# Optimization experiments

Measured on AMD Instinct MI355X. Metric: run time of the kernel, lower is better.

Reference implementation:

```python
import jax, jax.numpy as jnp
import numpy as np

P_DROP = 0.1
KEEP = 1.0 - P_DROP


def setup_inputs() -> dict:
    key = jax.random.key(0)
    ks = jax.random.split(key, 8)
    N, E, D, H, O, L = 50000, 800000, 128, 128, 64, 3
    x = jax.random.normal(ks[0], (N, D), dtype=jnp.float32)
    edge_index = jax.random.randint(ks[1], (2, E), 0, N, dtype=jnp.int64)
    s = 0.05  # weight scale for numeric stability
    Ws1 = jax.random.normal(ks[2], (L, D, H), dtype=jnp.float32) * s
    bs1 = jnp.zeros((L, H), dtype=jnp.float32)
    Ws2 = jax.random.normal(ks[3], (L, H, H), dtype=jnp.float32) * s
    bs2 = jnp.zeros((L, H), dtype=jnp.float32)
    Wlin = jax.random.normal(ks[4], (H, O), dtype=jnp.float32) * s
    blin = jnp.zeros((O,), dtype=jnp.float32)
    return {"x": x, "edge_index": edge_index, "Ws1": Ws1, "bs1": bs1,
            "Ws2": Ws2, "bs2": bs2, "Wlin": Wlin, "blin": blin}


def _gin_conv(x, src, dst, W1, b1, W2, b2, n_nodes):
    # GINConv (eps=0): h = MLP(x + sum_{j in N(i)} x_j)
    agg = jax.ops.segment_sum(x[src], dst, num_segments=n_nodes)  # [N, D]
    h = x + agg
    h = jax.nn.relu(h @ W1 + b1)
    h = jax.nn.relu(h @ W2 + b2)
    return h


def reference(x, edge_index, Ws1, bs1, Ws2, bs2, Wlin, blin):
    n_nodes = x.shape[0]
    src, dst = edge_index[0], edge_index[1]  # PyG flow: message from src to dst
    L = Ws1.shape[0]
    dkeys = jax.random.split(jax.random.key(42), L)
    h = x
    for l in range(L):
        h = _gin_conv(h, src, dst, Ws1[l], bs1[l], Ws2[l], bs2[l], n_nodes)
        h = jax.nn.relu(h)
        mask = jax.random.bernoulli(dkeys[l], KEEP, h.shape)
        h = jnp.where(mask, h / KEEP, 0.0)  # dropout p=0.1, training=True
    return h @ Wlin + blin
```

## Files before the change

kernel.cpp:

```cpp
#include <hip/hip_runtime.h>
#include <stdint.h>

typedef short short8 __attribute__((ext_vector_type(8)));
typedef float float4v __attribute__((ext_vector_type(4)));

__device__ static inline unsigned short f2bf(float f) {
  uint32_t u = __float_as_uint(f);
  u += 0x7fffu + ((u >> 16) & 1u);
  return (unsigned short)(u >> 16);
}
__device__ static inline float bf_lo(uint32_t v) { return __uint_as_float(v << 16); }
__device__ static inline float bf_hi(uint32_t v) { return __uint_as_float(v & 0xffff0000u); }

__host__ __device__ static inline void tf2x32(uint32_t k0, uint32_t k1,
                                              uint32_t x0, uint32_t x1,
                                              uint32_t* o0, uint32_t* o1) {
  const uint32_t ks2 = k0 ^ k1 ^ 0x1BD11BDAu;
  x0 += k0; x1 += k1;
#define TF_RND(r) { x0 += x1; x1 = (x1 << (r)) | (x1 >> (32 - (r))); x1 ^= x0; }
  TF_RND(13) TF_RND(15) TF_RND(26) TF_RND(6)
  x0 += k1;  x1 += ks2 + 1u;
  TF_RND(17) TF_RND(29) TF_RND(16) TF_RND(24)
  x0 += ks2; x1 += k0 + 2u;
  TF_RND(13) TF_RND(15) TF_RND(26) TF_RND(6)
  x0 += k0;  x1 += k1 + 3u;
  TF_RND(17) TF_RND(29) TF_RND(16) TF_RND(24)
  x0 += k1;  x1 += ks2 + 4u;
  TF_RND(13) TF_RND(15) TF_RND(26) TF_RND(6)
  x0 += ks2; x1 += k0 + 5u;
#undef TF_RND
  *o0 = x0; *o1 = x1;
}

__device__ static inline bool tf_keep(uint32_t k0, uint32_t k1, uint32_t idx) {
  uint32_t o0, o1;
  tf2x32(k0, k1, 0u, idx, &o0, &o1);
  const uint32_t bits = o0 ^ o1;
  const float u = __uint_as_float((bits >> 9) | 0x3f800000u) - 1.0f;
  return u < 0.9f;
}

__device__ static inline uint32_t mask_word(uint32_t k0, uint32_t k1, int b, int t) {
  const int wave = t >> 6, lane = t & 63;
  const int ch = wave & 1, rtw = wave >> 1;
  const int m = lane & 15, kg = lane >> 4;
  const int node0 = b * 64;
  uint32_t km = 0;
#pragma unroll
  for (int rt = 0; rt < 2; ++rt) {
#pragma unroll
    for (int nt = 0; nt < 4; ++nt) {
      const int col = ch * 64 + nt * 16 + m;
#pragma unroll
      for (int r = 0; r < 4; ++r) {
        const int ro = node0 + (rtw * 2 + rt) * 16 + kg * 4 + r;
        if (tf_keep(k0, k1, (uint32_t)ro * 128u + (uint32_t)col))
          km |= 1u << (rt * 16 + nt * 4 + r);
      }
    }
  }
  return km;
}

__global__ __launch_bounds__(256) void prep_kernel(
    const int* __restrict__ dst, int* __restrict__ count8, int N, int E,
    const float* __restrict__ x, unsigned short* __restrict__ xb,
    unsigned short* __restrict__ xb2, int n4,
    const float* __restrict__ Ws1, const float* __restrict__ Ws2,
    const float* __restrict__ Wlin, unsigned short* __restrict__ wpack,
    uint32_t* __restrict__ mask, int lblocks,
    uint32_t dk00, uint32_t dk01,
    int nCnt, int nConv, int nI) {
  const int t = threadIdx.x;
  const int g = blockIdx.x;
  if (g >= 10 * nI) {
    const int tid = (g - 10 * nI) * 256 + t;
    if (tid >= 13312) return;
    const float* W;
    int cols, r;
    size_t obase;
    if (tid < 12288) {
      const int mm = tid / 2048;
      r = tid % 2048;
      const int l = mm >> 1;
      W = (mm & 1) ? (Ws2 + (size_t)l * 16384) : (Ws1 + (size_t)l * 16384);
      cols = 128;
      obase = (size_t)mm * 16384;
    } else {
      r = tid - 12288;
      W = Wlin;
      cols = 64;
      obase = 6 * 16384;
    }
    const int ch = (cols == 128) ? (r >> 10) : 0;
    const int kt = (r >> 8) & 3;
    const int nt = (r >> 6) & 3;
    const int lane = r & 63;
    const int n = ch * 64 + nt * 16 + (lane & 15);
    const int kbase = kt * 32 + (lane >> 4) * 8;
    unsigned short o[8];
#pragma unroll
    for (int j = 0; j < 8; ++j) o[j] = f2bf(W[(size_t)(kbase + j) * cols + n]);
    uint4 ov;
    ov.x = (uint32_t)o[0] | ((uint32_t)o[1] << 16);
    ov.y = (uint32_t)o[2] | ((uint32_t)o[3] << 16);
    ov.z = (uint32_t)o[4] | ((uint32_t)o[5] << 16);
    ov.w = (uint32_t)o[6] | ((uint32_t)o[7] << 16);
    *(uint4*)(wpack + obase + ((size_t)((ch * 16 + kt * 4 + nt) * 64 + lane)) * 8) = ov;
    return;
  }
  const int cls = g % 10;
  const int j = g / 10;
  if (cls == 0) {
    if (j >= nCnt) return;
    const int tid = j * 256 + t;
    const int nt4 = (E + 3) >> 2;
    if (tid >= nt4) return;
    int* cseg = count8 + (size_t)(j & 7) * N;
    const int base = tid * 4;
    if (base + 4 <= E) {
      const int4 d4 = ((const int4*)dst)[tid];
      atomicAdd(&cseg[d4.x], 1);
      atomicAdd(&cseg[d4.y], 1);
      atomicAdd(&cseg[d4.z], 1);
      atomicAdd(&cseg[d4.w], 1);
    } else {
      for (int k = base; k < E; ++k) atomicAdd(&cseg[dst[k]], 1);
    }
    return;
  }
  if (cls == 9) {
    if (j >= lblocks) return;
    mask[(size_t)j * 256 + t] = mask_word(dk00, dk01, j, t);
    return;
  }
  const int cb = j * 8 + (cls - 1);
  if (cb >= nConv) return;
  const int i = cb * 256 + t;
  if (i < n4) {
    const float4 v = ((const float4*)x)[i];
    uint2 o;
    o.x = (uint32_t)f2bf(v.x) | ((uint32_t)f2bf(v.y) << 16);
    o.y = (uint32_t)f2bf(v.z) | ((uint32_t)f2bf(v.w) << 16);
    ((uint2*)xb)[i] = o;
  } else if (i < n4 + 32) {
    uint2 z; z.x = 0u; z.y = 0u;
    ((uint2*)xb)[i] = z;
    ((uint2*)xb2)[i] = z;
  }
}

__global__ __launch_bounds__(256) void scan1_kernel(
    const int* __restrict__ count8, int* __restrict__ bsum, int M8) {
  __shared__ int red[4];
  const int i = blockIdx.x * 256 + threadIdx.x;
  int v = (i < M8) ? count8[i] : 0;
  for (int off = 32; off > 0; off >>= 1) v += __shfl_down(v, off, 64);
  if ((threadIdx.x & 63) == 0) red[threadIdx.x >> 6] = v;
  __syncthreads();
  if (threadIdx.x == 0) bsum[blockIdx.x] = red[0] + red[1] + red[2] + red[3];
}

__global__ __launch_bounds__(256) void scan2_kernel(int* __restrict__ bsum, int nb) {
  __shared__ int buf[256];
  __shared__ int carry_s;
  const int t = threadIdx.x;
  if (t == 0) carry_s = 0;
  __syncthreads();
  for (int base = 0; base < nb; base += 256) {
    const int c = carry_s;
    const int i = base + t;
    const int v = (i < nb) ? bsum[i] : 0;
    __syncthreads();
    buf[t] = v;
    __syncthreads();
    for (int off = 1; off < 256; off <<= 1) {
      const int add = (t >= off) ? buf[t - off] : 0;
      __syncthreads();
      buf[t] += add;
      __syncthreads();
    }
    if (i < nb) bsum[i] = c + ((t == 0) ? 0 : buf[t - 1]);
    if (t == 0) carry_s = c + buf[255];
    __syncthreads();
  }
}

__global__ __launch_bounds__(256) void scan3_kernel(
    const int* __restrict__ count8, const int* __restrict__ bsum,
    int* __restrict__ cursor8, int M8) {
  __shared__ int buf[256];
  const int t = threadIdx.x;
  const int i = blockIdx.x * 256 + t;
  const int c = (i < M8) ? count8[i] : 0;
  buf[t] = c;
  __syncthreads();
  for (int off = 1; off < 256; off <<= 1) {
    const int add = (t >= off) ? buf[t - off] : 0;
    __syncthreads();
    buf[t] += add;
    __syncthreads();
  }
  if (i < M8) cursor8[i] = bsum[blockIdx.x] + buf[t] - c;
}

__global__ __launch_bounds__(256) void fill8_kernel(
    const int* __restrict__ src, const int* __restrict__ dst,
    int* __restrict__ cursor8, int* __restrict__ csr, int N, int E,
    uint32_t* __restrict__ mask, int lblocks,
    uint32_t dk10, uint32_t dk11, uint32_t dk20, uint32_t dk21, int nFill) {
  const int t = threadIdx.x;
  const int cls = blockIdx.x % 3;
  const int j = blockIdx.x / 3;
  if (cls == 0) {
    if (j >= nFill) return;
    const int tid = j * 256 + t;
    const int nt4 = (E + 3) >> 2;
    if (tid >= nt4) return;
    int* cseg = cursor8 + (size_t)(j & 7) * N;
    const int base = tid * 4;
    if (base + 4 <= E) {
      const int4 s4 = ((const int4*)src)[tid];
      const int4 d4 = ((const int4*)dst)[tid];
      const int p0 = atomicAdd(&cseg[d4.x], 1);
      const int p1 = atomicAdd(&cseg[d4.y], 1);
      const int p2 = atomicAdd(&cseg[d4.z], 1);
      const int p3 = atomicAdd(&cseg[d4.w], 1);
      csr[p0] = s4.x; csr[p1] = s4.y; csr[p2] = s4.z; csr[p3] = s4.w;
    } else {
      for (int k = base; k < E; ++k) {
        const int pos = atomicAdd(&cseg[dst[k]], 1);
        csr[pos] = src[k];
      }
    }
    return;
  }
  if (j >= lblocks) return;
  const uint32_t k0 = (cls == 1) ? dk10 : dk20;
  const uint32_t k1 = (cls == 1) ? dk11 : dk21;
  mask[(size_t)cls * lblocks * 256 + (size_t)j * 256 + t] = mask_word(k0, k1, j, t);
}

#define ACC16(vv, A0,A1,A2,A3,A4,A5,A6,A7)                         \
  A0 += bf_lo(vv.x); A1 += bf_hi(vv.x); A2 += bf_lo(vv.y); A3 += bf_hi(vv.y); \
  A4 += bf_lo(vv.z); A5 += bf_hi(vv.z); A6 += bf_lo(vv.w); A7 += bf_hi(vv.w);

__global__ __launch_bounds__(256, 3) void gin_layer_kernel(
    const unsigned short* __restrict__ hIn, unsigned short* __restrict__ hOut,
    const int* __restrict__ csr, const int* __restrict__ cursor8,
    const int* __restrict__ count8,
    const unsigned short* __restrict__ W1p, const float* __restrict__ b1,
    const unsigned short* __restrict__ W2p, const float* __restrict__ b2,
    const uint32_t* __restrict__ maskL, int N, int E) {
  __shared__ __align__(16) unsigned short agg[64 * 136];
  __shared__ __align__(16) unsigned short t1[64 * 136];
  const int t = threadIdx.x;
  const int q = t & 15;
  const int gb = (t & 63) & 48;
  const int node0 = blockIdx.x * 64;
  const uint4* hv = (const uint4*)hIn;

  for (int p = 0; p < 4; ++p) {
    const int nn = p * 16 + (t >> 4);
    const int node = node0 + nn;
    if (node < N) {
      int oe = 0, ol = 0;
      if (q < 8) {
        oe = cursor8[(size_t)q * N + node];
        ol = count8[(size_t)q * N + node];
      }
      int b0, b1s, b2s, b3s, b4s, b5s, b6s, b7s;
      int l0, l1, l2, l3, l4, l5, l6, l7;
      {
        int e;
        e = __shfl(oe, gb + 0, 64); l0 = __shfl(ol, gb + 0, 64); b0  = e - l0;
        e = __shfl(oe, gb + 1, 64); l1 = __shfl(ol, gb + 1, 64); b1s = e - l1;
        e = __shfl(oe, gb + 2, 64); l2 = __shfl(ol, gb + 2, 64); b2s = e - l2;
        e = __shfl(oe, gb + 3, 64); l3 = __shfl(ol, gb + 3, 64); b3s = e - l3;
        e = __shfl(oe, gb + 4, 64); l4 = __shfl(ol, gb + 4, 64); b4s = e - l4;
        e = __shfl(oe, gb + 5, 64); l5 = __shfl(ol, gb + 5, 64); b5s = e - l5;
        e = __shfl(oe, gb + 6, 64); l6 = __shfl(ol, gb + 6, 64); b6s = e - l6;
        e = __shfl(oe, gb + 7, 64); l7 = __shfl(ol, gb + 7, 64); b7s = e - l7;
      }
      const int c1 = l0, c2 = c1 + l1, c3 = c2 + l2, c4 = c3 + l3;
      const int c5 = c4 + l4, c6 = c5 + l5, c7 = c6 + l6, T = c7 + l7;

      const uint4 sv = hv[(size_t)node * 16 + q];
      float a0 = bf_lo(sv.x), a1 = bf_hi(sv.x), a2 = bf_lo(sv.y), a3 = bf_hi(sv.y);
      float a4 = bf_lo(sv.z), a5 = bf_hi(sv.z), a6 = bf_lo(sv.w), a7 = bf_hi(sv.w);
      float d0 = 0.f, d1 = 0.f, d2 = 0.f, d3 = 0.f, d4 = 0.f, d5 = 0.f, d6 = 0.f, d7 = 0.f;

      for (int base = 0; base < T; base += 16) {
        const int j = base + q;
        int pos = b0 + j;
        pos = (j >= c1) ? (b1s + j - c1) : pos;
        pos = (j >= c2) ? (b2s + j - c2) : pos;
        pos = (j >= c3) ? (b3s + j - c3) : pos;
        pos = (j >= c4) ? (b4s + j - c4) : pos;
        pos = (j >= c5) ? (b5s + j - c5) : pos;
        pos = (j >= c6) ? (b6s + j - c6) : pos;
        pos = (j >= c7) ? (b7s + j - c7) : pos;
        pos = (pos < E) ? pos : (E - 1);
        const int idx = (j < T) ? csr[pos] : N;
        uint4 v[16];
#pragma unroll
        for (int jj = 0; jj < 16; ++jj) {
          const int s = __shfl(idx, gb + jj, 64);
          v[jj] = hv[(size_t)s * 16 + q];
        }
#pragma unroll
        for (int jj = 0; jj < 16; jj += 2) {
          ACC16(v[jj], a0, a1, a2, a3, a4, a5, a6, a7)
          ACC16(v[jj + 1], d0, d1, d2, d3, d4, d5, d6, d7)
        }
      }
      a0 += d0; a1 += d1; a2 += d2; a3 += d3;
      a4 += d4; a5 += d5; a6 += d6; a7 += d7;

      uint4 ov;
      ov.x = (uint32_t)f2bf(a0) | ((uint32_t)f2bf(a1) << 16);
      ov.y = (uint32_t)f2bf(a2) | ((uint32_t)f2bf(a3) << 16);
      ov.z = (uint32_t)f2bf(a4) | ((uint32_t)f2bf(a5) << 16);
      ov.w = (uint32_t)f2bf(a6) | ((uint32_t)f2bf(a7) << 16);
      *(uint4*)(agg + (size_t)nn * 136 + q * 8) = ov;
    }
  }
  __syncthreads();

  const int wave = t >> 6, lane = t & 63;
  const int ch = wave & 1;
  const int rtw = wave >> 1;
  const int m = lane & 15, kg = lane >> 4;

  short8 bfrag[16];
  {
    const short8* wp = (const short8*)W1p + (size_t)(ch * 16) * 64 + lane;
#pragma unroll
    for (int i = 0; i < 16; ++i) bfrag[i] = wp[(size_t)i * 64];
  }
  float4v acc[2][4] = {};
#pragma unroll
  for (int rt = 0; rt < 2; ++rt) {
    const int lrow = (rtw * 2 + rt) * 16 + m;
#pragma unroll
    for (int kt = 0; kt < 4; ++kt) {
      const short8 af = *(const short8*)(agg + (size_t)lrow * 136 + kt * 32 + kg * 8);
#pragma unroll
      for (int nt = 0; nt < 4; ++nt)
        acc[rt][nt] = __builtin_amdgcn_mfma_f32_16x16x32_bf16(
            af, bfrag[kt * 4 + nt], acc[rt][nt], 0, 0, 0);
    }
  }
#pragma unroll
  for (int rt = 0; rt < 2; ++rt) {
#pragma unroll
    for (int nt = 0; nt < 4; ++nt) {
      const int col = ch * 64 + nt * 16 + m;
      const float bb = b1[col];
#pragma unroll
      for (int r = 0; r < 4; ++r) {
        const int lrow = (rtw * 2 + rt) * 16 + kg * 4 + r;
        float v = acc[rt][nt][r] + bb;
        v = fmaxf(v, 0.0f);
        t1[(size_t)lrow * 136 + col] = f2bf(v);
      }
    }
  }
  __syncthreads();

  {
    const short8* wp = (const short8*)W2p + (size_t)(ch * 16) * 64 + lane;
#pragma unroll
    for (int i = 0; i < 16; ++i) bfrag[i] = wp[(size_t)i * 64];
  }
  float4v acc2[2][4] = {};
#pragma unroll
  for (int rt = 0; rt < 2; ++rt) {
    const int lrow = (rtw * 2 + rt) * 16 + m;
#pragma unroll
    for (int kt = 0; kt < 4; ++kt) {
      const short8 af = *(const short8*)(t1 + (size_t)lrow * 136 + kt * 32 + kg * 8);
#pragma unroll
      for (int nt = 0; nt < 4; ++nt)
        acc2[rt][nt] = __builtin_amdgcn_mfma_f32_16x16x32_bf16(
            af, bfrag[kt * 4 + nt], acc2[rt][nt], 0, 0, 0);
    }
  }
  const uint32_t km = maskL[(size_t)blockIdx.x * 256 + t];
  const float KEEP_INV = 1.0f / 0.9f;
#pragma unroll
  for (int rt = 0; rt < 2; ++rt) {
#pragma unroll
    for (int nt = 0; nt < 4; ++nt) {
      const int col = ch * 64 + nt * 16 + m;
      const float bb = b2[col];
#pragma unroll
      for (int r = 0; r < 4; ++r) {
        const int lrow = (rtw * 2 + rt) * 16 + kg * 4 + r;
        float v = acc2[rt][nt][r] + bb;
        v = fmaxf(v, 0.0f);
        v = ((km >> (rt * 16 + nt * 4 + r)) & 1u) ? v * KEEP_INV : 0.0f;
        agg[(size_t)lrow * 136 + col] = f2bf(v);
      }
    }
  }
  __syncthreads();

  const int orow = t >> 2;
  const int oc0 = (t & 3) * 8;
  const int gnode = node0 + orow;
  if (gnode < N) {
#pragma unroll
    for (int i = 0; i < 4; ++i) {
      const uint4 vv = *(const uint4*)(agg + (size_t)orow * 136 + oc0 + i * 32);
      *(uint4*)(hOut + (size_t)gnode * 128 + oc0 + i * 32) = vv;
    }
  }
}

__global__ __launch_bounds__(256) void final_gemm_kernel(
    const unsigned short* __restrict__ A, const unsigned short* __restrict__ Wp,
    const float* __restrict__ bias, float* __restrict__ out, int M) {
  const int wave = threadIdx.x >> 6;
  const int lane = threadIdx.x & 63;
  const int m = lane & 15;
  const int kg = lane >> 4;

  short8 bfrag[16];
  const short8* wp = (const short8*)Wp + lane;
#pragma unroll
  for (int i = 0; i < 16; ++i) bfrag[i] = wp[(size_t)i * 64];

  const int row0 = blockIdx.x * 64 + wave * 16;
  const int arow = (row0 + m < M) ? (row0 + m) : (M - 1);
  const short8* ap = (const short8*)(A + (size_t)arow * 128 + kg * 8);

  short8 afrag[4];
#pragma unroll
  for (int kt = 0; kt < 4; ++kt) afrag[kt] = ap[kt * 4];

  float4v acc[4] = {};
#pragma unroll
  for (int kt = 0; kt < 4; ++kt) {
#pragma unroll
    for (int nt = 0; nt < 4; ++nt)
      acc[nt] = __builtin_amdgcn_mfma_f32_16x16x32_bf16(
          afrag[kt], bfrag[kt * 4 + nt], acc[nt], 0, 0, 0);
  }

#pragma unroll
  for (int nt = 0; nt < 4; ++nt) {
    const int col = nt * 16 + m;
    const float b = bias[col];
#pragma unroll
    for (int r = 0; r < 4; ++r) {
      const int ro = row0 + kg * 4 + r;
      if (ro >= M) continue;
      out[(size_t)ro * 64 + col] = acc[nt][r] + b;
    }
  }
}

extern "C" void kernel_launch(void* const* d_in, const int* in_sizes, int n_in,
                              void* d_out, int out_size, void* d_ws, size_t ws_size,
                              hipStream_t stream) {
  const float* x    = (const float*)d_in[0];
  const int*   ei   = (const int*)d_in[1];
  const float* Ws1  = (const float*)d_in[2];
  const float* bs1  = (const float*)d_in[3];
  const float* Ws2  = (const float*)d_in[4];
  const float* bs2  = (const float*)d_in[5];
  const float* Wlin = (const float*)d_in[6];
  const float* blin = (const float*)d_in[7];

  const int N = in_sizes[0] / 128;
  const int E = in_sizes[1] / 2;
  const int* src = ei;
  const int* dst = ei + E;
  const int M8 = 8 * N;
  const int lblocks = (N + 63) / 64;

  unsigned short* bufA  = (unsigned short*)d_ws;
  unsigned short* bufB  = bufA + (size_t)(N + 1) * 128;
  unsigned short* wpack = bufB + (size_t)(N + 1) * 128;
  int* count8  = (int*)(wpack + 106512);
  int* cursor8 = count8 + M8;
  int* csr     = cursor8 + M8;
  int* bsum    = csr + E;
  uint32_t* mask = (uint32_t*)(bsum + (M8 + 255) / 256 + 16);

  uint32_t dk[3][2];
  for (int l = 0; l < 3; ++l)
    tf2x32(0u, 42u, 0u, (uint32_t)l, &dk[l][0], &dk[l][1]);

  const int nt4 = (E + 3) / 4;
  const int eblocks = (nt4 + 255) / 256;
  const int nb8 = (M8 + 255) / 256;
  const int nconv = (N * 32 + 32 + 255) / 256;

  int nI = eblocks;
  if ((nconv + 7) / 8 > nI) nI = (nconv + 7) / 8;
  if (lblocks > nI) nI = lblocks;

  hipMemsetAsync(count8, 0, (size_t)M8 * sizeof(int), stream);
  prep_kernel<<<10 * nI + 52, 256, 0, stream>>>(
      dst, count8, N, E, x, bufA, bufB, N * 32, Ws1, Ws2, Wlin, wpack,
      mask, lblocks, dk[0][0], dk[0][1], eblocks, nconv, nI);
  scan1_kernel<<<nb8, 256, 0, stream>>>(count8, bsum, M8);
  scan2_kernel<<<1, 256, 0, stream>>>(bsum, nb8);
  scan3_kernel<<<nb8, 256, 0, stream>>>(count8, bsum, cursor8, M8);
  const int fI = (eblocks > lblocks) ? eblocks : lblocks;
  fill8_kernel<<<3 * fI, 256, 0, stream>>>(
      src, dst, cursor8, csr, N, E, mask, lblocks,
      dk[1][0], dk[1][1], dk[2][0], dk[2][1], eblocks);

  unsigned short* hin = bufA;
  unsigned short* hout = bufB;
  for (int l = 0; l < 3; ++l) {
    gin_layer_kernel<<<lblocks, 256, 0, stream>>>(
        hin, hout, csr, cursor8, count8,
        wpack + (size_t)(l * 2) * 16384, bs1 + (size_t)l * 128,
        wpack + (size_t)(l * 2 + 1) * 16384, bs2 + (size_t)l * 128,
        mask + (size_t)l * lblocks * 256, N, E);
    unsigned short* tmp = hin; hin = hout; hout = tmp;
  }

  final_gemm_kernel<<<lblocks, 256, 0, stream>>>(
      hin, wpack + 6 * 16384, blin, (float*)d_out, N);
}
```

Before: 296.5 us.

## Halve GIN layer tile to 32 nodes and rebalance prep/mask work across kernels

Each GIN layer block now handles 32 nodes instead of 64. LDS and per-wave accumulators are halved so launch bounds can request 6 blocks per CU, giving better latency hiding for the gather-heavy aggregation. The dropout mask layout shrinks to match. Layer-0 mask generation moves from the prep kernel into the scan1 kernel, and prep/fill grids are re-interleaved so the different work types overlap better. The cost is that weight fragments are loaded once per 32 nodes instead of 64, and the block-index mapping is more intricate.

```diff
diff --git a/kernel.cpp b/kernel.cpp
--- a/kernel.cpp
+++ b/kernel.cpp
@@ -42,21 +42,18 @@
 
 __device__ static inline uint32_t mask_word(uint32_t k0, uint32_t k1, int b, int t) {
   const int wave = t >> 6, lane = t & 63;
-  const int ch = wave & 1, rtw = wave >> 1;
+  const int rt = wave >> 1, ch = wave & 1;
   const int m = lane & 15, kg = lane >> 4;
-  const int node0 = b * 64;
+  const int node0 = b * 32;
   uint32_t km = 0;
 #pragma unroll
-  for (int rt = 0; rt < 2; ++rt) {
-#pragma unroll
-    for (int nt = 0; nt < 4; ++nt) {
-      const int col = ch * 64 + nt * 16 + m;
-#pragma unroll
-      for (int r = 0; r < 4; ++r) {
-        const int ro = node0 + (rtw * 2 + rt) * 16 + kg * 4 + r;
-        if (tf_keep(k0, k1, (uint32_t)ro * 128u + (uint32_t)col))
-          km |= 1u << (rt * 16 + nt * 4 + r);
-      }
+  for (int nt = 0; nt < 4; ++nt) {
+    const int col = ch * 64 + nt * 16 + m;
+#pragma unroll
+    for (int r = 0; r < 4; ++r) {
+      const int ro = node0 + rt * 16 + kg * 4 + r;
+      if (tf_keep(k0, k1, (uint32_t)ro * 128u + (uint32_t)col))
+        km |= 1u << (nt * 4 + r);
     }
   }
   return km;
@@ -68,97 +65,102 @@
     unsigned short* __restrict__ xb2, int n4,
     const float* __restrict__ Ws1, const float* __restrict__ Ws2,
     const float* __restrict__ Wlin, unsigned short* __restrict__ wpack,
-    uint32_t* __restrict__ mask, int lblocks,
-    uint32_t dk00, uint32_t dk01,
-    int nCnt, int nConv, int nI) {
+    int nCnt, int nConv, int interA) {
   const int t = threadIdx.x;
   const int g = blockIdx.x;
-  if (g >= 10 * nI) {
-    const int tid = (g - 10 * nI) * 256 + t;
-    if (tid >= 13312) return;
-    const float* W;
-    int cols, r;
-    size_t obase;
-    if (tid < 12288) {
-      const int mm = tid / 2048;
-      r = tid % 2048;
-      const int l = mm >> 1;
-      W = (mm & 1) ? (Ws2 + (size_t)l * 16384) : (Ws1 + (size_t)l * 16384);
-      cols = 128;
-      obase = (size_t)mm * 16384;
-    } else {
-      r = tid - 12288;
-      W = Wlin;
-      cols = 64;
-      obase = 6 * 16384;
-    }
-    const int ch = (cols == 128) ? (r >> 10) : 0;
-    const int kt = (r >> 8) & 3;
-    const int nt = (r >> 6) & 3;
-    const int lane = r & 63;
-    const int n = ch * 64 + nt * 16 + (lane & 15);
-    const int kbase = kt * 32 + (lane >> 4) * 8;
-    unsigned short o[8];
-#pragma unroll
-    for (int j = 0; j < 8; ++j) o[j] = f2bf(W[(size_t)(kbase + j) * cols + n]);
-    uint4 ov;
-    ov.x = (uint32_t)o[0] | ((uint32_t)o[1] << 16);
-    ov.y = (uint32_t)o[2] | ((uint32_t)o[3] << 16);
-    ov.z = (uint32_t)o[4] | ((uint32_t)o[5] << 16);
-    ov.w = (uint32_t)o[6] | ((uint32_t)o[7] << 16);
-    *(uint4*)(wpack + obase + ((size_t)((ch * 16 + kt * 4 + nt) * 64 + lane)) * 8) = ov;
+  int c;
+  if (g < interA) {
+    const int m = g >> 4, s = g & 15;
+    if (s < 8) {
+      const int j = m * 8 + s;
+      if (j >= nCnt) return;
+      const int tid = j * 256 + t;
+      const int nt4 = (E + 3) >> 2;
+      if (tid >= nt4) return;
+      int* cseg = count8 + (size_t)(j & 7) * N;
+      const int base = tid * 4;
+      if (base + 4 <= E) {
+        const int4 d4 = ((const int4*)dst)[tid];
+        atomicAdd(&cseg[d4.x], 1);
+        atomicAdd(&cseg[d4.y], 1);
+        atomicAdd(&cseg[d4.z], 1);
+        atomicAdd(&cseg[d4.w], 1);
+      } else {
+        for (int k = base; k < E; ++k) atomicAdd(&cseg[dst[k]], 1);
+      }
+      return;
+    }
+    c = m * 8 + (s - 8);
+  } else {
+    c = (interA >> 1) + (g - interA);
+  }
+  if (c < nConv) {
+    const int i = c * 256 + t;
+    if (i < n4) {
+      const float4 v = ((const float4*)x)[i];
+      uint2 o;
+      o.x = (uint32_t)f2bf(v.x) | ((uint32_t)f2bf(v.y) << 16);
+      o.y = (uint32_t)f2bf(v.z) | ((uint32_t)f2bf(v.w) << 16);
+      ((uint2*)xb)[i] = o;
+    } else if (i < n4 + 32) {
+      uint2 z; z.x = 0u; z.y = 0u;
+      ((uint2*)xb)[i] = z;
+      ((uint2*)xb2)[i] = z;
+    }
     return;
   }
-  const int cls = g % 10;
-  const int j = g / 10;
-  if (cls == 0) {
-    if (j >= nCnt) return;
-    const int tid = j * 256 + t;
-    const int nt4 = (E + 3) >> 2;
-    if (tid >= nt4) return;
-    int* cseg = count8 + (size_t)(j & 7) * N;
-    const int base = tid * 4;
-    if (base + 4 <= E) {
-      const int4 d4 = ((const int4*)dst)[tid];
-      atomicAdd(&cseg[d4.x], 1);
-      atomicAdd(&cseg[d4.y], 1);
-      atomicAdd(&cseg[d4.z], 1);
-      atomicAdd(&cseg[d4.w], 1);
-    } else {
-      for (int k = base; k < E; ++k) atomicAdd(&cseg[dst[k]], 1);
-    }
+  const int tid = (c - nConv) * 256 + t;
+  if (tid >= 13312) return;
+  const float* W;
+  int cols, r;
+  size_t obase;
+  if (tid < 12288) {
+    const int mm = tid / 2048;
+    r = tid % 2048;
+    const int l = mm >> 1;
+    W = (mm & 1) ? (Ws2 + (size_t)l * 16384) : (Ws1 + (size_t)l * 16384);
+    cols = 128;
+    obase = (size_t)mm * 16384;
+  } else {
+    r = tid - 12288;
+    W = Wlin;
+    cols = 64;
+    obase = 6 * 16384;
+  }
+  const int ch = (cols == 128) ? (r >> 10) : 0;
+  const int kt = (r >> 8) & 3;
+  const int nt = (r >> 6) & 3;
+  const int lane = r & 63;
+  const int n = ch * 64 + nt * 16 + (lane & 15);
+  const int kbase = kt * 32 + (lane >> 4) * 8;
+  unsigned short o[8];
+#pragma unroll
+  for (int j = 0; j < 8; ++j) o[j] = f2bf(W[(size_t)(kbase + j) * cols + n]);
+  uint4 ov;
+  ov.x = (uint32_t)o[0] | ((uint32_t)o[1] << 16);
+  ov.y = (uint32_t)o[2] | ((uint32_t)o[3] << 16);
+  ov.z = (uint32_t)o[4] | ((uint32_t)o[5] << 16);
+  ov.w = (uint32_t)o[6] | ((uint32_t)o[7] << 16);
+  *(uint4*)(wpack + obase + ((size_t)((ch * 16 + kt * 4 + nt) * 64 + lane)) * 8) = ov;
+}
+
+__global__ __launch_bounds__(256) void scan1_kernel(
+    const int* __restrict__ count8, int* __restrict__ bsum, int M8,
+    uint32_t* __restrict__ mask, int mblocks, uint32_t dk00, uint32_t dk01) {
+  const int t = threadIdx.x;
+  if (blockIdx.x & 1) {
+    const int j = blockIdx.x >> 1;
+    if (j < mblocks) mask[(size_t)j * 256 + t] = mask_word(dk00, dk01, j, t);
     return;
   }
-  if (cls == 9) {
-    if (j >= lblocks) return;
-    mask[(size_t)j * 256 + t] = mask_word(dk00, dk01, j, t);
-    return;
-  }
-  const int cb = j * 8 + (cls - 1);
-  if (cb >= nConv) return;
-  const int i = cb * 256 + t;
-  if (i < n4) {
-    const float4 v = ((const float4*)x)[i];
-    uint2 o;
-    o.x = (uint32_t)f2bf(v.x) | ((uint32_t)f2bf(v.y) << 16);
-    o.y = (uint32_t)f2bf(v.z) | ((uint32_t)f2bf(v.w) << 16);
-    ((uint2*)xb)[i] = o;
-  } else if (i < n4 + 32) {
-    uint2 z; z.x = 0u; z.y = 0u;
-    ((uint2*)xb)[i] = z;
-    ((uint2*)xb2)[i] = z;
-  }
-}
-
-__global__ __launch_bounds__(256) void scan1_kernel(
-    const int* __restrict__ count8, int* __restrict__ bsum, int M8) {
   __shared__ int red[4];
-  const int i = blockIdx.x * 256 + threadIdx.x;
+  const int blk = blockIdx.x >> 1;
+  const int i = blk * 256 + t;
   int v = (i < M8) ? count8[i] : 0;
   for (int off = 32; off > 0; off >>= 1) v += __shfl_down(v, off, 64);
-  if ((threadIdx.x & 63) == 0) red[threadIdx.x >> 6] = v;
+  if ((t & 63) == 0) red[t >> 6] = v;
   __syncthreads();
-  if (threadIdx.x == 0) bsum[blockIdx.x] = red[0] + red[1] + red[2] + red[3];
+  if (t == 0) bsum[blk] = red[0] + red[1] + red[2] + red[3];
 }
 
 __global__ __launch_bounds__(256) void scan2_kernel(int* __restrict__ bsum, int nb) {
@@ -207,12 +209,12 @@
 __global__ __launch_bounds__(256) void fill8_kernel(
     const int* __restrict__ src, const int* __restrict__ dst,
     int* __restrict__ cursor8, int* __restrict__ csr, int N, int E,
-    uint32_t* __restrict__ mask, int lblocks,
+    uint32_t* __restrict__ mask, int mblocks,
     uint32_t dk10, uint32_t dk11, uint32_t dk20, uint32_t dk21, int nFill) {
   const int t = threadIdx.x;
-  const int cls = blockIdx.x % 3;
-  const int j = blockIdx.x / 3;
-  if (cls == 0) {
+  const int m = blockIdx.x / 40, s = blockIdx.x % 40;
+  if (s < 8) {
+    const int j = m * 8 + s;
     if (j >= nFill) return;
     const int tid = j * 256 + t;
     const int nt4 = (E + 3) >> 2;
@@ -235,32 +237,36 @@
     }
     return;
   }
-  if (j >= lblocks) return;
-  const uint32_t k0 = (cls == 1) ? dk10 : dk20;
-  const uint32_t k1 = (cls == 1) ? dk11 : dk21;
-  mask[(size_t)cls * lblocks * 256 + (size_t)j * 256 + t] = mask_word(k0, k1, j, t);
+  const int k = m * 32 + (s - 8);
+  if (k >= 2 * mblocks) return;
+  const int lay2 = (k >= mblocks);
+  const int j = lay2 ? (k - mblocks) : k;
+  const uint32_t k0 = lay2 ? dk20 : dk10;
+  const uint32_t k1 = lay2 ? dk21 : dk11;
+  mask[(size_t)(1 + lay2) * mblocks * 256 + (size_t)j * 256 + t] =
+      mask_word(k0, k1, j, t);
 }
 
 #define ACC16(vv, A0,A1,A2,A3,A4,A5,A6,A7)                         \
   A0 += bf_lo(vv.x); A1 += bf_hi(vv.x); A2 += bf_lo(vv.y); A3 += bf_hi(vv.y); \
   A4 += bf_lo(vv.z); A5 += bf_hi(vv.z); A6 += bf_lo(vv.w); A7 += bf_hi(vv.w);
 
-__global__ __launch_bounds__(256, 3) void gin_layer_kernel(
+__global__ __launch_bounds__(256, 6) void gin_layer_kernel(
     const unsigned short* __restrict__ hIn, unsigned short* __restrict__ hOut,
     const int* __restrict__ csr, const int* __restrict__ cursor8,
     const int* __restrict__ count8,
     const unsigned short* __restrict__ W1p, const float* __restrict__ b1,
     const unsigned short* __restrict__ W2p, const float* __restrict__ b2,
     const uint32_t* __restrict__ maskL, int N, int E) {
-  __shared__ __align__(16) unsigned short agg[64 * 136];
-  __shared__ __align__(16) unsigned short t1[64 * 136];
+  __shared__ __align__(16) unsigned short agg[32 * 136];
+  __shared__ __align__(16) unsigned short t1[32 * 136];
   const int t = threadIdx.x;
   const int q = t & 15;
   const int gb = (t & 63) & 48;
-  const int node0 = blockIdx.x * 64;
+  const int node0 = blockIdx.x * 32;
   const uint4* hv = (const uint4*)hIn;
 
-  for (int p = 0; p < 4; ++p) {
+  for (int p = 0; p < 2; ++p) {
     const int nn = p * 16 + (t >> 4);
     const int node = node0 + nn;
     if (node < N) {
@@ -328,8 +334,7 @@
   __syncthreads();
 
   const int wave = t >> 6, lane = t & 63;
-  const int ch = wave & 1;
-  const int rtw = wave >> 1;
+  const int rt = wave >> 1, ch = wave & 1;
   const int m = lane & 15, kg = lane >> 4;
 
   short8 bfrag[16];
@@ -338,32 +343,25 @@
 #pragma unroll
     for (int i = 0; i < 16; ++i) bfrag[i] = wp[(size_t)i * 64];
   }
-  float4v acc[2][4] = {};
-#pragma unroll
-  for (int rt = 0; rt < 2; ++rt) {
-    const int lrow = (rtw * 2 + rt) * 16 + m;
-#pragma unroll
-    for (int kt = 0; kt < 4; ++kt) {
-      const short8 af = *(const short8*)(agg + (size_t)lrow * 136 + kt * 32 + kg * 8);
-#pragma unroll
-      for (int nt = 0; nt < 4; ++nt)
-        acc[rt][nt] = __builtin_amdgcn_mfma_f32_16x16x32_bf16(
-            af, bfrag[kt * 4 + nt], acc[rt][nt], 0, 0, 0);
-    }
-  }
-#pragma unroll
-  for (int rt = 0; rt < 2; ++rt) {
-#pragma unroll
-    for (int nt = 0; nt < 4; ++nt) {
-      const int col = ch * 64 + nt * 16 + m;
-      const float bb = b1[col];
-#pragma unroll
-      for (int r = 0; r < 4; ++r) {
-        const int lrow = (rtw * 2 + rt) * 16 + kg * 4 + r;
-        float v = acc[rt][nt][r] + bb;
-        v = fmaxf(v, 0.0f);
-        t1[(size_t)lrow * 136 + col] = f2bf(v);
-      }
+  float4v acc[4] = {};
+#pragma unroll
+  for (int kt = 0; kt < 4; ++kt) {
+    const short8 af = *(const short8*)(agg + (size_t)(rt * 16 + m) * 136 + kt * 32 + kg * 8);
+#pragma unroll
+    for (int nt = 0; nt < 4; ++nt)
+      acc[nt] = __builtin_amdgcn_mfma_f32_16x16x32_bf16(
+          af, bfrag[kt * 4 + nt], acc[nt], 0, 0, 0);
+  }
+#pragma unroll
+  for (int nt = 0; nt < 4; ++nt) {
+    const int col = ch * 64 + nt * 16 + m;
+    const float bb = b1[col];
+#pragma unroll
+    for (int r = 0; r < 4; ++r) {
+      const int lrow = rt * 16 + kg * 4 + r;
+      float v = acc[nt][r] + bb;
+      v = fmaxf(v, 0.0f);
+      t1[(size_t)lrow * 136 + col] = f2bf(v);
     }
   }
   __syncthreads();
@@ -373,47 +371,40 @@
 #pragma unroll
     for (int i = 0; i < 16; ++i) bfrag[i] = wp[(size_t)i * 64];
   }
-  float4v acc2[2][4] = {};
-#pragma unroll
-  for (int rt = 0; rt < 2; ++rt) {
-    const int lrow = (rtw * 2 + rt) * 16 + m;
-#pragma unroll
-    for (int kt = 0; kt < 4; ++kt) {
-      const short8 af = *(const short8*)(t1 + (size_t)lrow * 136 + kt * 32 + kg * 8);
-#pragma unroll
-      for (int nt = 0; nt < 4; ++nt)
-        acc2[rt][nt] = __builtin_amdgcn_mfma_f32_16x16x32_bf16(
-            af, bfrag[kt * 4 + nt], acc2[rt][nt], 0, 0, 0);
-    }
+  float4v acc2[4] = {};
+#pragma unroll
+  for (int kt = 0; kt < 4; ++kt) {
+    const short8 af = *(const short8*)(t1 + (size_t)(rt * 16 + m) * 136 + kt * 32 + kg * 8);
+#pragma unroll
+    for (int nt = 0; nt < 4; ++nt)
+      acc2[nt] = __builtin_amdgcn_mfma_f32_16x16x32_bf16(
+          af, bfrag[kt * 4 + nt], acc2[nt], 0, 0, 0);
   }
   const uint32_t km = maskL[(size_t)blockIdx.x * 256 + t];
   const float KEEP_INV = 1.0f / 0.9f;
 #pragma unroll
-  for (int rt = 0; rt < 2; ++rt) {
-#pragma unroll
-    for (int nt = 0; nt < 4; ++nt) {
-      const int col = ch * 64 + nt * 16 + m;
-      const float bb = b2[col];
-#pragma unroll
-      for (int r = 0; r < 4; ++r) {
-        const int lrow = (rtw * 2 + rt) * 16 + kg * 4 + r;
-        float v = acc2[rt][nt][r] + bb;
-        v = fmaxf(v, 0.0f);
-        v = ((km >> (rt * 16 + nt * 4 + r)) & 1u) ? v * KEEP_INV : 0.0f;
-        agg[(size_t)lrow * 136 + col] = f2bf(v);
-      }
+  for (int nt = 0; nt < 4; ++nt) {
+    const int col = ch * 64 + nt * 16 + m;
+    const float bb = b2[col];
+#pragma unroll
+    for (int r = 0; r < 4; ++r) {
+      const int lrow = rt * 16 + kg * 4 + r;
+      float v = acc2[nt][r] + bb;
+      v = fmaxf(v, 0.0f);
+      v = ((km >> (nt * 4 + r)) & 1u) ? v * KEEP_INV : 0.0f;
+      agg[(size_t)lrow * 136 + col] = f2bf(v);
     }
   }
   __syncthreads();
 
-  const int orow = t >> 2;
-  const int oc0 = (t & 3) * 8;
+  const int orow = t >> 3;
+  const int oc0 = (t & 7) * 16;
   const int gnode = node0 + orow;
   if (gnode < N) {
 #pragma unroll
-    for (int i = 0; i < 4; ++i) {
-      const uint4 vv = *(const uint4*)(agg + (size_t)orow * 136 + oc0 + i * 32);
-      *(uint4*)(hOut + (size_t)gnode * 128 + oc0 + i * 32) = vv;
+    for (int i = 0; i < 2; ++i) {
+      const uint4 vv = *(const uint4*)(agg + (size_t)orow * 136 + oc0 + i * 8);
+      *(uint4*)(hOut + (size_t)gnode * 128 + oc0 + i * 8) = vv;
     }
   }
 }
@@ -478,7 +469,7 @@
   const int* src = ei;
   const int* dst = ei + E;
   const int M8 = 8 * N;
-  const int lblocks = (N + 63) / 64;
+  const int mblocks = (N + 31) / 32;
 
   unsigned short* bufA  = (unsigned short*)d_ws;
   unsigned short* bufB  = bufA + (size_t)(N + 1) * 128;
@@ -498,33 +489,35 @@
   const int nb8 = (M8 + 255) / 256;
   const int nconv = (N * 32 + 32 + 255) / 256;
 
-  int nI = eblocks;
-  if ((nconv + 7) / 8 > nI) nI = (nconv + 7) / 8;
-  if (lblocks > nI) nI = lblocks;
+  const int P1 = (eblocks + 7) / 8;
+  const int interA = P1 * 16;
+  const int convInSlots = P1 * 8;
+  const int prep_grid = interA + (nconv - convInSlots) + 52;
 
   hipMemsetAsync(count8, 0, (size_t)M8 * sizeof(int), stream);
-  prep_kernel<<<10 * nI + 52, 256, 0, stream>>>(
+  prep_kernel<<<prep_grid, 256, 0, stream>>>(
       dst, count8, N, E, x, bufA, bufB, N * 32, Ws1, Ws2, Wlin, wpack,
-      mask, lblocks, dk[0][0], dk[0][1], eblocks, nconv, nI);
-  scan1_kernel<<<nb8, 256, 0, stream>>>(count8, bsum, M8);
+      eblocks, nconv, interA);
+  scan1_kernel<<<2 * nb8, 256, 0, stream>>>(count8, bsum, M8, mask, mblocks,
+                                            dk[0][0], dk[0][1]);
   scan2_kernel<<<1, 256, 0, stream>>>(bsum, nb8);
   scan3_kernel<<<nb8, 256, 0, stream>>>(count8, bsum, cursor8, M8);
-  const int fI = (eblocks > lblocks) ? eblocks : lblocks;
-  fill8_kernel<<<3 * fI, 256, 0, stream>>>(
-      src, dst, cursor8, csr, N, E, mask, lblocks,
+  const int fill_grid = P1 * 40;
+  fill8_kernel<<<fill_grid, 256, 0, stream>>>(
+      src, dst, cursor8, csr, N, E, mask, mblocks,
       dk[1][0], dk[1][1], dk[2][0], dk[2][1], eblocks);
 
   unsigned short* hin = bufA;
   unsigned short* hout = bufB;
   for (int l = 0; l < 3; ++l) {
-    gin_layer_kernel<<<lblocks, 256, 0, stream>>>(
+    gin_layer_kernel<<<mblocks, 256, 0, stream>>>(
         hin, hout, csr, cursor8, count8,
         wpack + (size_t)(l * 2) * 16384, bs1 + (size_t)l * 128,
         wpack + (size_t)(l * 2 + 1) * 16384, bs2 + (size_t)l * 128,
-        mask + (size_t)l * lblocks * 256, N, E);
+        mask + (size_t)l * mblocks * 256, N, E);
     unsigned short* tmp = hin; hin = hout; hout = tmp;
   }
 
-  final_gemm_kernel<<<lblocks, 256, 0, stream>>>(
+  final_gemm_kernel<<<(N + 63) / 64, 256, 0, stream>>>(
       hin, wpack + 6 * 16384, blin, (float*)d_out, N);
 }
```

New measurement: 418.5 us. 41.2% more time.

## Rebalance preprocessing work mix across prep, scan1 and fill kernels

Applied to the files above, without the earlier changes.

Moves the layer-0 dropout mask generation out of the prep kernel into the scan1 kernel, interleaving mask blocks with the reduction blocks. Prep and fill grids are re-laid out so blocks are packed in fixed ratios (8 count blocks to 64 convert blocks, 8 fill blocks to 32 mask blocks) rather than padding every class to the largest block count. The goal is fewer idle early-exit blocks and better overlap of the compute-heavy Threefry mask work with the atomic-bound counting and scatter phases. Correctness depends on the new grid sizes covering every mask and convert block, since the mask coverage in scan1 is bounded by 2*nb8 blocks.

```diff
diff --git a/kernel.cpp b/kernel.cpp
--- a/kernel.cpp
+++ b/kernel.cpp
@@ -68,97 +68,98 @@
     unsigned short* __restrict__ xb2, int n4,
     const float* __restrict__ Ws1, const float* __restrict__ Ws2,
     const float* __restrict__ Wlin, unsigned short* __restrict__ wpack,
-    uint32_t* __restrict__ mask, int lblocks,
-    uint32_t dk00, uint32_t dk01,
-    int nCnt, int nConv, int nI) {
+    int nCnt, int nConv, int interA) {
   const int t = threadIdx.x;
   const int g = blockIdx.x;
-  if (g >= 10 * nI) {
-    const int tid = (g - 10 * nI) * 256 + t;
-    if (tid >= 13312) return;
-    const float* W;
-    int cols, r;
-    size_t obase;
-    if (tid < 12288) {
-      const int mm = tid / 2048;
-      r = tid % 2048;
-      const int l = mm >> 1;
-      W = (mm & 1) ? (Ws2 + (size_t)l * 16384) : (Ws1 + (size_t)l * 16384);
-      cols = 128;
-      obase = (size_t)mm * 16384;
-    } else {
-      r = tid - 12288;
-      W = Wlin;
-      cols = 64;
-      obase = 6 * 16384;
-    }
-    const int ch = (cols == 128) ? (r >> 10) : 0;
-    const int kt = (r >> 8) & 3;
-    const int nt = (r >> 6) & 3;
-    const int lane = r & 63;
-    const int n = ch * 64 + nt * 16 + (lane & 15);
-    const int kbase = kt * 32 + (lane >> 4) * 8;
-    unsigned short o[8];
-#pragma unroll
-    for (int j = 0; j < 8; ++j) o[j] = f2bf(W[(size_t)(kbase + j) * cols + n]);
-    uint4 ov;
-    ov.x = (uint32_t)o[0] | ((uint32_t)o[1] << 16);
-    ov.y = (uint32_t)o[2] | ((uint32_t)o[3] << 16);
-    ov.z = (uint32_t)o[4] | ((uint32_t)o[5] << 16);
-    ov.w = (uint32_t)o[6] | ((uint32_t)o[7] << 16);
-    *(uint4*)(wpack + obase + ((size_t)((ch * 16 + kt * 4 + nt) * 64 + lane)) * 8) = ov;
+  if (g < interA) {
+    const int m = g / 72, s = g % 72;
+    if (s < 8) {
+      const int j = m * 8 + s;
+      if (j >= nCnt) return;
+      const int tid = j * 256 + t;
+      const int nt4 = (E + 3) >> 2;
+      if (tid >= nt4) return;
+      int* cseg = count8 + (size_t)(j & 7) * N;
+      const int base = tid * 4;
+      if (base + 4 <= E) {
+        const int4 d4 = ((const int4*)dst)[tid];
+        atomicAdd(&cseg[d4.x], 1);
+        atomicAdd(&cseg[d4.y], 1);
+        atomicAdd(&cseg[d4.z], 1);
+        atomicAdd(&cseg[d4.w], 1);
+      } else {
+        for (int k = base; k < E; ++k) atomicAdd(&cseg[dst[k]], 1);
+      }
+      return;
+    }
+    const int c = m * 64 + (s - 8);
+    if (c >= nConv) return;
+    const int i = c * 256 + t;
+    if (i < n4) {
+      const float4 v = ((const float4*)x)[i];
+      uint2 o;
+      o.x = (uint32_t)f2bf(v.x) | ((uint32_t)f2bf(v.y) << 16);
+      o.y = (uint32_t)f2bf(v.z) | ((uint32_t)f2bf(v.w) << 16);
+      ((uint2*)xb)[i] = o;
+    } else if (i < n4 + 32) {
+      uint2 z; z.x = 0u; z.y = 0u;
+      ((uint2*)xb)[i] = z;
+      ((uint2*)xb2)[i] = z;
+    }
     return;
   }
-  const int cls = g % 10;
-  const int j = g / 10;
-  if (cls == 0) {
-    if (j >= nCnt) return;
-    const int tid = j * 256 + t;
-    const int nt4 = (E + 3) >> 2;
-    if (tid >= nt4) return;
-    int* cseg = count8 + (size_t)(j & 7) * N;
-    const int base = tid * 4;
-    if (base + 4 <= E) {
-      const int4 d4 = ((const int4*)dst)[tid];
-      atomicAdd(&cseg[d4.x], 1);
-      atomicAdd(&cseg[d4.y], 1);
-      atomicAdd(&cseg[d4.z], 1);
-      atomicAdd(&cseg[d4.w], 1);
-    } else {
-      for (int k = base; k < E; ++k) atomicAdd(&cseg[dst[k]], 1);
-    }
+  const int tid = (g - interA) * 256 + t;
+  if (tid >= 13312) return;
+  const float* W;
+  int cols, r;
+  size_t obase;
+  if (tid < 12288) {
+    const int mm = tid / 2048;
+    r = tid % 2048;
+    const int l = mm >> 1;
+    W = (mm & 1) ? (Ws2 + (size_t)l * 16384) : (Ws1 + (size_t)l * 16384);
+    cols = 128;
+    obase = (size_t)mm * 16384;
+  } else {
+    r = tid - 12288;
+    W = Wlin;
+    cols = 64;
+    obase = 6 * 16384;
+  }
+  const int ch = (cols == 128) ? (r >> 10) : 0;
+  const int kt = (r >> 8) & 3;
+  const int nt = (r >> 6) & 3;
+  const int lane = r & 63;
+  const int n = ch * 64 + nt * 16 + (lane & 15);
+  const int kbase = kt * 32 + (lane >> 4) * 8;
+  unsigned short o[8];
+#pragma unroll
+  for (int j = 0; j < 8; ++j) o[j] = f2bf(W[(size_t)(kbase + j) * cols + n]);
+  uint4 ov;
+  ov.x = (uint32_t)o[0] | ((uint32_t)o[1] << 16);
+  ov.y = (uint32_t)o[2] | ((uint32_t)o[3] << 16);
+  ov.z = (uint32_t)o[4] | ((uint32_t)o[5] << 16);
+  ov.w = (uint32_t)o[6] | ((uint32_t)o[7] << 16);
+  *(uint4*)(wpack + obase + ((size_t)((ch * 16 + kt * 4 + nt) * 64 + lane)) * 8) = ov;
+}
+
+__global__ __launch_bounds__(256) void scan1_kernel(
+    const int* __restrict__ count8, int* __restrict__ bsum, int M8,
+    uint32_t* __restrict__ mask, int mblocks, uint32_t dk00, uint32_t dk01) {
+  const int t = threadIdx.x;
+  if (blockIdx.x & 1) {
+    const int j = blockIdx.x >> 1;
+    if (j < mblocks) mask[(size_t)j * 256 + t] = mask_word(dk00, dk01, j, t);
     return;
   }
-  if (cls == 9) {
-    if (j >= lblocks) return;
-    mask[(size_t)j * 256 + t] = mask_word(dk00, dk01, j, t);
-    return;
-  }
-  const int cb = j * 8 + (cls - 1);
-  if (cb >= nConv) return;
-  const int i = cb * 256 + t;
-  if (i < n4) {
-    const float4 v = ((const float4*)x)[i];
-    uint2 o;
-    o.x = (uint32_t)f2bf(v.x) | ((uint32_t)f2bf(v.y) << 16);
-    o.y = (uint32_t)f2bf(v.z) | ((uint32_t)f2bf(v.w) << 16);
-    ((uint2*)xb)[i] = o;
-  } else if (i < n4 + 32) {
-    uint2 z; z.x = 0u; z.y = 0u;
-    ((uint2*)xb)[i] = z;
-    ((uint2*)xb2)[i] = z;
-  }
-}
-
-__global__ __launch_bounds__(256) void scan1_kernel(
-    const int* __restrict__ count8, int* __restrict__ bsum, int M8) {
   __shared__ int red[4];
-  const int i = blockIdx.x * 256 + threadIdx.x;
+  const int blk = blockIdx.x >> 1;
+  const int i = blk * 256 + t;
   int v = (i < M8) ? count8[i] : 0;
   for (int off = 32; off > 0; off >>= 1) v += __shfl_down(v, off, 64);
-  if ((threadIdx.x & 63) == 0) red[threadIdx.x >> 6] = v;
+  if ((t & 63) == 0) red[t >> 6] = v;
   __syncthreads();
-  if (threadIdx.x == 0) bsum[blockIdx.x] = red[0] + red[1] + red[2] + red[3];
+  if (t == 0) bsum[blk] = red[0] + red[1] + red[2] + red[3];
 }
 
 __global__ __launch_bounds__(256) void scan2_kernel(int* __restrict__ bsum, int nb) {
@@ -207,12 +208,12 @@
 __global__ __launch_bounds__(256) void fill8_kernel(
     const int* __restrict__ src, const int* __restrict__ dst,
     int* __restrict__ cursor8, int* __restrict__ csr, int N, int E,
-    uint32_t* __restrict__ mask, int lblocks,
+    uint32_t* __restrict__ mask, int mblocks,
     uint32_t dk10, uint32_t dk11, uint32_t dk20, uint32_t dk21, int nFill) {
   const int t = threadIdx.x;
-  const int cls = blockIdx.x % 3;
-  const int j = blockIdx.x / 3;
-  if (cls == 0) {
+  const int m = blockIdx.x / 40, s = blockIdx.x % 40;
+  if (s < 8) {
+    const int j = m * 8 + s;
     if (j >= nFill) return;
     const int tid = j * 256 + t;
     const int nt4 = (E + 3) >> 2;
@@ -235,10 +236,14 @@
     }
     return;
   }
-  if (j >= lblocks) return;
-  const uint32_t k0 = (cls == 1) ? dk10 : dk20;
-  const uint32_t k1 = (cls == 1) ? dk11 : dk21;
-  mask[(size_t)cls * lblocks * 256 + (size_t)j * 256 + t] = mask_word(k0, k1, j, t);
+  const int k = m * 32 + (s - 8);
+  if (k >= 2 * mblocks) return;
+  const int lay2 = (k >= mblocks);
+  const int j = lay2 ? (k - mblocks) : k;
+  const uint32_t k0 = lay2 ? dk20 : dk10;
+  const uint32_t k1 = lay2 ? dk21 : dk11;
+  mask[(size_t)(1 + lay2) * mblocks * 256 + (size_t)j * 256 + t] =
+      mask_word(k0, k1, j, t);
 }
 
 #define ACC16(vv, A0,A1,A2,A3,A4,A5,A6,A7)                         \
@@ -498,19 +503,19 @@
   const int nb8 = (M8 + 255) / 256;
   const int nconv = (N * 32 + 32 + 255) / 256;
 
-  int nI = eblocks;
-  if ((nconv + 7) / 8 > nI) nI = (nconv + 7) / 8;
-  if (lblocks > nI) nI = lblocks;
+  const int P1 = (eblocks + 7) / 8;
+  const int interA = P1 * 72;
+  const int prep_grid = interA + 52;
 
   hipMemsetAsync(count8, 0, (size_t)M8 * sizeof(int), stream);
-  prep_kernel<<<10 * nI + 52, 256, 0, stream>>>(
+  prep_kernel<<<prep_grid, 256, 0, stream>>>(
       dst, count8, N, E, x, bufA, bufB, N * 32, Ws1, Ws2, Wlin, wpack,
-      mask, lblocks, dk[0][0], dk[0][1], eblocks, nconv, nI);
-  scan1_kernel<<<nb8, 256, 0, stream>>>(count8, bsum, M8);
+      eblocks, nconv, interA);
+  scan1_kernel<<<2 * nb8, 256, 0, stream>>>(count8, bsum, M8, mask, lblocks,
+                                            dk[0][0], dk[0][1]);
   scan2_kernel<<<1, 256, 0, stream>>>(bsum, nb8);
   scan3_kernel<<<nb8, 256, 0, stream>>>(count8, bsum, cursor8, M8);
-  const int fI = (eblocks > lblocks) ? eblocks : lblocks;
-  fill8_kernel<<<3 * fI, 256, 0, stream>>>(
+  fill8_kernel<<<P1 * 40, 256, 0, stream>>>(
       src, dst, cursor8, csr, N, E, mask, lblocks,
       dk[1][0], dk[1][1], dk[2][0], dk[2][1], eblocks);
 
```

After: 325.7 us. 9.9% more time.
